# Optimization experiments

Hardware: AMD Instinct MI355X
Metric: run time of the kernel (lower is better)

## Reference

```python
import jax, jax.numpy as jnp
import numpy as np

N_NODES = 100000


def _gcn_conv(x, W, b, src, dst, n_nodes):
    # PyG GCNConv: out = D^-1/2 (A+I) D^-1/2 (x W) + b, self-loops already in (src,dst)
    h = x @ W  # [N, out]
    deg = jax.ops.segment_sum(jnp.ones(dst.shape, x.dtype), dst, num_segments=n_nodes)
    dis = jax.lax.rsqrt(jnp.maximum(deg, 1.0)) * (deg > 0)  # deg>=1 due to self-loops
    norm = dis[src] * dis[dst]  # [E]
    msg = h[src] * norm[:, None]  # gather + scale
    return jax.ops.segment_sum(msg, dst, num_segments=n_nodes) + b


def setup_inputs() -> dict:
    key = jax.random.key(0)
    ks = jax.random.split(key, 8)
    nfeat, nhid, nclasses = 128, 128, 40
    n, e = N_NODES, 1600000
    x = jax.random.normal(ks[0], (n, nfeat), dtype=jnp.float32)
    edge_index = jax.random.randint(ks[1], (2, e), 0, n, dtype=jnp.int64)
    # Glorot-ish init for weights
    W1 = jax.random.normal(ks[2], (nfeat, nhid), dtype=jnp.float32) / np.sqrt(nfeat)
    b1 = jnp.zeros((nhid,), dtype=jnp.float32)
    W2 = jax.random.normal(ks[3], (nhid, nhid), dtype=jnp.float32) / np.sqrt(nhid)
    b2 = jnp.zeros((nhid,), dtype=jnp.float32)
    Wl = jax.random.normal(ks[4], (nhid, nclasses), dtype=jnp.float32) / np.sqrt(nhid)
    bl = jnp.zeros((nclasses,), dtype=jnp.float32)
    return {"x": x, "edge_index": edge_index, "W1": W1, "b1": b1,
            "W2": W2, "b2": b2, "Wl": Wl, "bl": bl}


def reference(x, edge_index, W1, b1, W2, b2, Wl, bl):
    n = x.shape[0]
    # add self-loops (PyG GCNConv default add_self_loops=True)
    loops = jnp.arange(n, dtype=edge_index.dtype)
    src = jnp.concatenate([edge_index[0], loops])
    dst = jnp.concatenate([edge_index[1], loops])
    h = jax.nn.relu(_gcn_conv(x, W1, b1, src, dst, n))
    h = jax.nn.relu(_gcn_conv(h, W2, b2, src, dst, n))
    return h @ Wl + bl
```

## Files before the change

### kernel.cpp

```cpp
#include <hip/hip_runtime.h>


typedef _Float16 half_t;
typedef int   v4i __attribute__((ext_vector_type(4)));
union H4 { short4 s; half_t h[4]; };
union H8 { v4i v; half_t h[8]; };

static __device__ __forceinline__ float4 ld4(const float* p) {
    return *reinterpret_cast<const float4*>(p);
}
static __device__ __forceinline__ short4 ldh4(const half_t* p) {
    return *reinterpret_cast<const short4*>(p);
}
static __device__ __forceinline__ v4i nt_ld4i(const int* p) {
    return __builtin_nontemporal_load(reinterpret_cast<const v4i*>(p));
}

__global__ void init_kernel(int* __restrict__ deg, int* __restrict__ cursor, int n) {
    int i = blockIdx.x * blockDim.x + threadIdx.x;
    if (i < n) { deg[i] = 1; cursor[i] = 0; }
}

__global__ void hist_kernel(const int* __restrict__ dstv, int* __restrict__ deg, int e) {
    int i4 = (blockIdx.x * blockDim.x + threadIdx.x) * 4;
    if (i4 + 3 < e) {
        v4i d = nt_ld4i(dstv + i4);
        atomicAdd(&deg[d.x], 1); atomicAdd(&deg[d.y], 1);
        atomicAdd(&deg[d.z], 1); atomicAdd(&deg[d.w], 1);
    } else {
        for (int k = i4; k < e; ++k) atomicAdd(&deg[__builtin_nontemporal_load(dstv + k)], 1);
    }
}

__global__ void scan_block_sum(const int* __restrict__ deg, int* __restrict__ bsums,
                               float* __restrict__ dis, int n) {
    __shared__ int s[256];
    int i = blockIdx.x * 256 + threadIdx.x;
    int v = (i < n) ? (deg[i] - 1) : 0;
    if (i < n) dis[i] = rsqrtf((float)deg[i]);
    s[threadIdx.x] = v;
    __syncthreads();
    for (int o = 128; o > 0; o >>= 1) {
        if (threadIdx.x < o) s[threadIdx.x] += s[threadIdx.x + o];
        __syncthreads();
    }
    if (threadIdx.x == 0) bsums[blockIdx.x] = s[0];
}

__global__ void scan_bsums(const int* __restrict__ bsums, int* __restrict__ bexcl, int nb) {
    __shared__ int s[512];
    int t = threadIdx.x;
    int v = (t < nb) ? bsums[t] : 0;
    s[t] = v; __syncthreads();
    for (int o = 1; o < 512; o <<= 1) {
        int x = (t >= o) ? s[t - o] : 0;
        __syncthreads();
        s[t] += x;
        __syncthreads();
    }
    if (t < nb) bexcl[t] = s[t] - v;
}

__global__ void scan_offsets(const int* __restrict__ deg, const int* __restrict__ bexcl,
                             int* __restrict__ offs, int n) {
    __shared__ int s[256];
    int t = threadIdx.x;
    int i = blockIdx.x * 256 + t;
    int v = (i < n) ? (deg[i] - 1) : 0;
    s[t] = v; __syncthreads();
    for (int o = 1; o < 256; o <<= 1) {
        int x = (t >= o) ? s[t - o] : 0;
        __syncthreads();
        s[t] += x;
        __syncthreads();
    }
    if (i < n) offs[i] = bexcl[blockIdx.x] + s[t] - v;
}

__global__ void scatter_kernel(const int* __restrict__ srcv, const int* __restrict__ dstv,
                               const int* __restrict__ offs, int* __restrict__ cursor,
                               int* __restrict__ csr, int e) {
    int i4 = (blockIdx.x * blockDim.x + threadIdx.x) * 4;
    if (i4 + 3 < e) {
        v4i sv = nt_ld4i(srcv + i4);
        v4i dv = nt_ld4i(dstv + i4);
        int p;
        p = offs[dv.x] + atomicAdd(&cursor[dv.x], 1); __builtin_nontemporal_store(sv.x, csr + p);
        p = offs[dv.y] + atomicAdd(&cursor[dv.y], 1); __builtin_nontemporal_store(sv.y, csr + p);
        p = offs[dv.z] + atomicAdd(&cursor[dv.z], 1); __builtin_nontemporal_store(sv.z, csr + p);
        p = offs[dv.w] + atomicAdd(&cursor[dv.w], 1); __builtin_nontemporal_store(sv.w, csr + p);
    } else {
        for (int k = i4; k < e; ++k) {
            int d = __builtin_nontemporal_load(dstv + k);
            int p = offs[d] + atomicAdd(&cursor[d], 1);
            __builtin_nontemporal_store(__builtin_nontemporal_load(srcv + k), csr + p);
        }
    }
}

template <typename AT>
__global__ __launch_bounds__(1024, 1)
void gemm_nn128(const AT* __restrict__ A, const float* __restrict__ W,
                const float* __restrict__ rowscale, half_t* __restrict__ out,
                int n, int nchunk) {
    __shared__ float Ws[128 * 128];
    __shared__ float As[128 * 128];
    constexpr bool HALF = (sizeof(AT) == 2);
    int tid = threadIdx.x;
#pragma unroll
    for (int q = 0; q < 4; ++q)
        ((float4*)Ws)[tid + 1024 * q] = ((const float4*)W)[tid + 1024 * q];

    int tc = tid & 31;
    int tr = tid >> 5;
    int col0 = tc * 4;

    v4i pf[4];
    auto prefetch = [&](int cc) {
        if constexpr (HALF) {
#pragma unroll
            for (int q = 0; q < 2; ++q) {
                int u = tid + 1024 * q;
                int row = cc * 128 + (u >> 4);
                if (row > n - 1) row = n - 1;
                pf[q] = nt_ld4i((const int*)((const half_t*)A + (size_t)row * 128 + (u & 15) * 8));
            }
        } else {
#pragma unroll
            for (int q = 0; q < 4; ++q) {
                int fidx = tid + 1024 * q;
                int row = cc * 128 + (fidx >> 5);
                if (row > n - 1) row = n - 1;
                pf[q] = nt_ld4i((const int*)((const float*)A + (size_t)row * 128 + (fidx & 31) * 4));
            }
        }
    };

    int c = blockIdx.x;
    if (c < nchunk) prefetch(c);
    for (; c < nchunk; c += gridDim.x) {
        __syncthreads();
        if constexpr (HALF) {
#pragma unroll
            for (int q = 0; q < 2; ++q) {
                int u = tid + 1024 * q;
                int r = u >> 4, cc = (u & 15) * 8;
                H8 hh; hh.v = pf[q];
#pragma unroll
                for (int j = 0; j < 8; ++j) As[r * 128 + cc + j] = (float)hh.h[j];
            }
        } else {
#pragma unroll
            for (int q = 0; q < 4; ++q)
                ((v4i*)As)[tid + 1024 * q] = pf[q];
        }
        __syncthreads();
        if (c + (int)gridDim.x < nchunk) prefetch(c + gridDim.x);
        float4 acc[4];
#pragma unroll
        for (int r = 0; r < 4; ++r) acc[r] = make_float4(0.f, 0.f, 0.f, 0.f);
#pragma unroll 8
        for (int k4 = 0; k4 < 32; ++k4) {
            float4 av[4], wv[4];
#pragma unroll
            for (int r = 0; r < 4; ++r)
                av[r] = ld4(&As[(tr * 4 + r) * 128 + k4 * 4]);
#pragma unroll
            for (int kk = 0; kk < 4; ++kk)
                wv[kk] = ld4(&Ws[(k4 * 4 + kk) * 128 + col0]);
#pragma unroll
            for (int r = 0; r < 4; ++r) {
                acc[r].x += av[r].x * wv[0].x + av[r].y * wv[1].x + av[r].z * wv[2].x + av[r].w * wv[3].x;
                acc[r].y += av[r].x * wv[0].y + av[r].y * wv[1].y + av[r].z * wv[2].y + av[r].w * wv[3].y;
                acc[r].z += av[r].x * wv[0].z + av[r].y * wv[1].z + av[r].z * wv[2].z + av[r].w * wv[3].z;
                acc[r].w += av[r].x * wv[0].w + av[r].y * wv[1].w + av[r].z * wv[2].w + av[r].w * wv[3].w;
            }
        }
#pragma unroll
        for (int r = 0; r < 4; ++r) {
            int row = c * 128 + tr * 4 + r;
            if (row < n) {
                float s = rowscale[row];
                H4 o;
                o.h[0] = (half_t)(acc[r].x * s); o.h[1] = (half_t)(acc[r].y * s);
                o.h[2] = (half_t)(acc[r].z * s); o.h[3] = (half_t)(acc[r].w * s);
                *reinterpret_cast<short4*>(out + (size_t)row * 128 + col0) = o.s;
            }
        }
    }
}

__global__ __launch_bounds__(256)
void agg_kernel(const half_t* __restrict__ hs, const float* __restrict__ dis,
                const int* __restrict__ offs, const int* __restrict__ deg,
                const int* __restrict__ csr, const float* __restrict__ bias,
                half_t* __restrict__ out, int n, int etot) {
    int node = blockIdx.x * 8 + (threadIdx.x >> 5);
    if (node >= n) return;
    int lane = threadIdx.x & 31;
    int l4 = lane * 4;
    float di = dis[node];
    H4 sv; sv.s = ldh4(hs + (size_t)node * 128 + l4);
    float4 acc;
    acc.x = (float)sv.h[0]; acc.y = (float)sv.h[1];
    acc.z = (float)sv.h[2]; acc.w = (float)sv.h[3];
    int st = offs[node];
    int cnt = deg[node] - 1;
    auto clampn = [&](int s) { return ((unsigned)s >= (unsigned)n) ? 0 : s; };
    for (int base = 0; base < cnt; base += 32) {
        int ii = st + base + lane;
        int iv = __builtin_nontemporal_load(csr + (ii < etot ? ii : etot - 1));
        int m = cnt - base; m = m > 32 ? 32 : m;
        int e = 0;
        for (; e + 4 <= m; e += 4) {
            int s0 = clampn(__shfl(iv, e, 32)),     s1 = clampn(__shfl(iv, e + 1, 32));
            int s2 = clampn(__shfl(iv, e + 2, 32)), s3 = clampn(__shfl(iv, e + 3, 32));
            H4 v0, v1, v2, v3;
            v0.s = ldh4(hs + (size_t)s0 * 128 + l4);
            v1.s = ldh4(hs + (size_t)s1 * 128 + l4);
            v2.s = ldh4(hs + (size_t)s2 * 128 + l4);
            v3.s = ldh4(hs + (size_t)s3 * 128 + l4);
            acc.x += ((float)v0.h[0] + (float)v1.h[0]) + ((float)v2.h[0] + (float)v3.h[0]);
            acc.y += ((float)v0.h[1] + (float)v1.h[1]) + ((float)v2.h[1] + (float)v3.h[1]);
            acc.z += ((float)v0.h[2] + (float)v1.h[2]) + ((float)v2.h[2] + (float)v3.h[2]);
            acc.w += ((float)v0.h[3] + (float)v1.h[3]) + ((float)v2.h[3] + (float)v3.h[3]);
        }
        for (; e < m; ++e) {
            int s0 = clampn(__shfl(iv, e, 32));
            H4 v0; v0.s = ldh4(hs + (size_t)s0 * 128 + l4);
            acc.x += (float)v0.h[0]; acc.y += (float)v0.h[1];
            acc.z += (float)v0.h[2]; acc.w += (float)v0.h[3];
        }
    }
    float4 b = ld4(bias + l4);
    float ox = fmaxf(acc.x * di + b.x, 0.f);
    float oy = fmaxf(acc.y * di + b.y, 0.f);
    float oz = fmaxf(acc.z * di + b.z, 0.f);
    float ow = fmaxf(acc.w * di + b.w, 0.f);
    H4 o;
    o.h[0] = (half_t)ox; o.h[1] = (half_t)oy; o.h[2] = (half_t)oz; o.h[3] = (half_t)ow;
    *reinterpret_cast<short4*>(out + (size_t)node * 128 + l4) = o.s;
}

__global__ __launch_bounds__(256)
void head_kernel(const half_t* __restrict__ A, const float* __restrict__ W,
                 const float* __restrict__ bias, float* __restrict__ out, int n) {
    __shared__ float Ws[128 * 40];
    __shared__ float bs[40];
    int tid = threadIdx.x;
#pragma unroll
    for (int q = 0; q < 5; ++q)
        ((float4*)Ws)[tid + 256 * q] = ((const float4*)W)[tid + 256 * q];
    if (tid < 40) bs[tid] = bias[tid];
    __syncthreads();

    int rg = tid >> 3;
    int c0 = (tid & 7) * 5;
    int row0 = blockIdx.x * 64 + rg * 2;
    int rA = row0 < n ? row0 : n - 1;
    int rB = row0 + 1 < n ? row0 + 1 : n - 1;
    float acc[2][5];
#pragma unroll
    for (int r = 0; r < 2; ++r)
#pragma unroll
        for (int cc = 0; cc < 5; ++cc) acc[r][cc] = 0.f;
#pragma unroll 4
    for (int k4 = 0; k4 < 32; ++k4) {
        H4 a0, a1;
        a0.s = ldh4(A + (size_t)rA * 128 + k4 * 4);
        a1.s = ldh4(A + (size_t)rB * 128 + k4 * 4);
#pragma unroll
        for (int kk = 0; kk < 4; ++kk) {
            int k = k4 * 4 + kk;
            float f0 = (float)a0.h[kk], f1 = (float)a1.h[kk];
#pragma unroll
            for (int cc = 0; cc < 5; ++cc) {
                float w = Ws[k * 40 + c0 + cc];
                acc[0][cc] += f0 * w;
                acc[1][cc] += f1 * w;
            }
        }
    }
#pragma unroll
    for (int r = 0; r < 2; ++r) {
        int row = row0 + r;
        if (row < n) {
#pragma unroll
            for (int cc = 0; cc < 5; ++cc)
                out[(size_t)row * 40 + c0 + cc] = acc[r][cc] + bs[c0 + cc];
        }
    }
}

extern "C" void kernel_launch(void* const* d_in, const int* in_sizes, int n_in,
                              void* d_out, int out_size, void* d_ws, size_t ws_size,
                              hipStream_t stream) {
    const float* x  = (const float*)d_in[0];
    const int*   ei = (const int*)d_in[1];
    const float* W1 = (const float*)d_in[2];
    const float* b1 = (const float*)d_in[3];
    const float* W2 = (const float*)d_in[4];
    const float* b2 = (const float*)d_in[5];
    const float* Wl = (const float*)d_in[6];
    const float* bl = (const float*)d_in[7];
    float* out = (float*)d_out;

    int n = in_sizes[0] / 128;
    int e = in_sizes[1] / 2;
    const int* srcv = ei;
    const int* dstv = ei + e;

    char* p = (char*)d_ws;
    auto carve = [&](size_t bytes) { char* r = p; p += (bytes + 255) & ~(size_t)255; return r; };
    int*    deg    = (int*)   carve((size_t)n * 4);
    float*  dis    = (float*) carve((size_t)n * 4);
    int*    offs   = (int*)   carve((size_t)n * 4);
    int*    cursor = (int*)   carve((size_t)n * 4);
    int*    bsums  = (int*)   carve(512 * 4);
    int*    bexcl  = (int*)   carve(512 * 4);
    int*    csr    = (int*)   carve((size_t)e * 4);
    half_t* bufA   = (half_t*)carve((size_t)n * 128 * 2);
    half_t* bufB   = (half_t*)carve((size_t)n * 128 * 2);

    int nb = (n + 255) / 256;
    int nchunk = (n + 127) / 128;
    int e4b = (e / 4 + 255) / 256 + 1;

    hipLaunchKernelGGL(init_kernel, dim3((n + 255) / 256), dim3(256), 0, stream, deg, cursor, n);
    hipLaunchKernelGGL(hist_kernel, dim3(e4b), dim3(256), 0, stream, dstv, deg, e);
    hipLaunchKernelGGL(scan_block_sum, dim3(nb), dim3(256), 0, stream, deg, bsums, dis, n);
    hipLaunchKernelGGL(scan_bsums, dim3(1), dim3(512), 0, stream, bsums, bexcl, nb);
    hipLaunchKernelGGL(scan_offsets, dim3(nb), dim3(256), 0, stream, deg, bexcl, offs, n);
    hipLaunchKernelGGL(scatter_kernel, dim3(e4b), dim3(256), 0, stream,
                       srcv, dstv, offs, cursor, csr, e);

    hipLaunchKernelGGL(gemm_nn128<float>, dim3(256), dim3(1024), 0, stream,
                       x, W1, dis, bufA, n, nchunk);
    hipLaunchKernelGGL(agg_kernel, dim3((n + 7) / 8), dim3(256), 0, stream,
                       bufA, dis, offs, deg, csr, b1, bufB, n, e);
    hipLaunchKernelGGL(gemm_nn128<half_t>, dim3(256), dim3(1024), 0, stream,
                       bufB, W2, dis, bufA, n, nchunk);
    hipLaunchKernelGGL(agg_kernel, dim3((n + 7) / 8), dim3(256), 0, stream,
                       bufA, dis, offs, deg, csr, b2, bufB, n, e);
    hipLaunchKernelGGL(head_kernel, dim3((n + 63) / 64), dim3(256), 0, stream,
                       bufB, Wl, bl, out, n);
}
```

Before: 549.0 us.

## Bucket CSR scatter writes into position-range buffers before final placement

The single random-write scatter into the CSR array becomes two passes. The first pass appends (position, src) pairs into per-bucket staging lists covering 16K-slot position ranges, replicated 8 ways by block index and stored in the reused bufA workspace. The second pass has one block per bucket write its pairs into csr, so writes land in a localized range and cache better. The cost is an extra atomic per edge on the bucket counters, double the traffic for staged pairs, and an extra kernel launch; pairs that overflow a bucket's capacity fall back to a direct write.

After: 879.0 us. 1.6x slower.

```diff
diff --git a/kernel.cpp b/kernel.cpp
--- a/kernel.cpp
+++ b/kernel.cpp
@@ -6,6 +6,9 @@
 union H4 { short4 s; half_t h[4]; };
 union H8 { v4i v; half_t h[8]; };
 
+#define BKSHIFT 14
+#define BKCAP   2560
+
 static __device__ __forceinline__ float4 ld4(const float* p) {
     return *reinterpret_cast<const float4*>(p);
 }
@@ -16,9 +19,11 @@
     return __builtin_nontemporal_load(reinterpret_cast<const v4i*>(p));
 }
 
-__global__ void init_kernel(int* __restrict__ deg, int* __restrict__ cursor, int n) {
+__global__ void init_kernel(int* __restrict__ deg, int* __restrict__ cursor,
+                            int* __restrict__ bcnt, int n) {
     int i = blockIdx.x * blockDim.x + threadIdx.x;
     if (i < n) { deg[i] = 1; cursor[i] = 0; }
+    if (i < 1024) bcnt[i] = 0;
 }
 
 __global__ void hist_kernel(const int* __restrict__ dstv, int* __restrict__ deg, int e) {
@@ -77,23 +82,39 @@
     if (i < n) offs[i] = bexcl[blockIdx.x] + s[t] - v;
 }
 
-__global__ void scatter_kernel(const int* __restrict__ srcv, const int* __restrict__ dstv,
-                               const int* __restrict__ offs, int* __restrict__ cursor,
-                               int* __restrict__ csr, int e) {
+__global__ void scatter_pass1(const int* __restrict__ srcv, const int* __restrict__ dstv,
+                              const int* __restrict__ offs, int* __restrict__ cursor,
+                              int* __restrict__ bcnt, int2* __restrict__ bbuf,
+                              int* __restrict__ csr, int e) {
+    int xp = (blockIdx.x & 7) << 7;
     int i4 = (blockIdx.x * blockDim.x + threadIdx.x) * 4;
+    auto emit = [&](int d, int s) {
+        int pos = offs[d] + atomicAdd(&cursor[d], 1);
+        int b = xp + (pos >> BKSHIFT);
+        int slot = atomicAdd(&bcnt[b], 1);
+        if (slot < BKCAP) bbuf[(size_t)b * BKCAP + slot] = make_int2(pos, s);
+        else csr[pos] = s;
+    };
     if (i4 + 3 < e) {
         v4i sv = nt_ld4i(srcv + i4);
         v4i dv = nt_ld4i(dstv + i4);
-        int p;
-        p = offs[dv.x] + atomicAdd(&cursor[dv.x], 1); __builtin_nontemporal_store(sv.x, csr + p);
-        p = offs[dv.y] + atomicAdd(&cursor[dv.y], 1); __builtin_nontemporal_store(sv.y, csr + p);
-        p = offs[dv.z] + atomicAdd(&cursor[dv.z], 1); __builtin_nontemporal_store(sv.z, csr + p);
-        p = offs[dv.w] + atomicAdd(&cursor[dv.w], 1); __builtin_nontemporal_store(sv.w, csr + p);
+        emit(dv.x, sv.x); emit(dv.y, sv.y); emit(dv.z, sv.z); emit(dv.w, sv.w);
     } else {
-        for (int k = i4; k < e; ++k) {
-            int d = __builtin_nontemporal_load(dstv + k);
-            int p = offs[d] + atomicAdd(&cursor[d], 1);
-            __builtin_nontemporal_store(__builtin_nontemporal_load(srcv + k), csr + p);
+        for (int k = i4; k < e; ++k)
+            emit(__builtin_nontemporal_load(dstv + k), __builtin_nontemporal_load(srcv + k));
+    }
+}
+
+__global__ void scatter_pass2(const int2* __restrict__ bbuf, const int* __restrict__ bcnt,
+                              int* __restrict__ csr) {
+    int b = blockIdx.x;
+    for (int xp = 0; xp < 8; ++xp) {
+        int idx = (xp << 7) + b;
+        int cnt = bcnt[idx]; if (cnt > BKCAP) cnt = BKCAP;
+        const int2* lst = bbuf + (size_t)idx * BKCAP;
+        for (int t = threadIdx.x; t < cnt; t += 256) {
+            int2 pr = lst[t];
+            csr[pr.x] = pr.y;
         }
     }
 }
@@ -318,21 +339,26 @@
     int*    cursor = (int*)   carve((size_t)n * 4);
     int*    bsums  = (int*)   carve(512 * 4);
     int*    bexcl  = (int*)   carve(512 * 4);
+    int*    bcnt   = (int*)   carve(1024 * 4);
     int*    csr    = (int*)   carve((size_t)e * 4);
     half_t* bufA   = (half_t*)carve((size_t)n * 128 * 2);
     half_t* bufB   = (half_t*)carve((size_t)n * 128 * 2);
+    int2*   bbuf   = (int2*)bufA;
 
     int nb = (n + 255) / 256;
     int nchunk = (n + 127) / 128;
     int e4b = (e / 4 + 255) / 256 + 1;
-
-    hipLaunchKernelGGL(init_kernel, dim3((n + 255) / 256), dim3(256), 0, stream, deg, cursor, n);
+    int nbuck = (e + (1 << BKSHIFT) - 1) >> BKSHIFT;
+
+    hipLaunchKernelGGL(init_kernel, dim3((n + 255) / 256), dim3(256), 0, stream,
+                       deg, cursor, bcnt, n);
     hipLaunchKernelGGL(hist_kernel, dim3(e4b), dim3(256), 0, stream, dstv, deg, e);
     hipLaunchKernelGGL(scan_block_sum, dim3(nb), dim3(256), 0, stream, deg, bsums, dis, n);
     hipLaunchKernelGGL(scan_bsums, dim3(1), dim3(512), 0, stream, bsums, bexcl, nb);
     hipLaunchKernelGGL(scan_offsets, dim3(nb), dim3(256), 0, stream, deg, bexcl, offs, n);
-    hipLaunchKernelGGL(scatter_kernel, dim3(e4b), dim3(256), 0, stream,
-                       srcv, dstv, offs, cursor, csr, e);
+    hipLaunchKernelGGL(scatter_pass1, dim3(e4b), dim3(256), 0, stream,
+                       srcv, dstv, offs, cursor, bcnt, bbuf, csr, e);
+    hipLaunchKernelGGL(scatter_pass2, dim3(nbuck), dim3(256), 0, stream, bbuf, bcnt, csr);
 
     hipLaunchKernelGGL(gemm_nn128<float>, dim3(256), dim3(1024), 0, stream,
                        x, W1, dis, bufA, n, nchunk);
```
